# Kernel optimization log

Measured on AMD Instinct MI355X. Metric: run time of the kernel, lower is better.

The kernel has to match this reference:

```python
import jax, jax.numpy as jnp
import numpy as np

N_NODES = 100000
N_EDGES = 3200000
N_FEAT = 500
N_HID = 256
N_CLASS = 40


def spmm(edge_row, edge_col, edge_val, x, num_nodes):
    # out[i] = sum_{e: row[e]==i} val[e] * x[col[e]]
    msgs = edge_val[:, None] * x[edge_col]          # [E, F] gather + scale
    return jax.ops.segment_sum(msgs, edge_row, num_segments=num_nodes)


def setup_inputs() -> dict:
    key = jax.random.key(0)
    k1, k2, k3, k4, k5, k6, k7, k8 = jax.random.split(key, 8)
    features = jax.random.normal(k1, (N_NODES, N_FEAT), dtype=jnp.float32)
    edge_row = jax.random.randint(k2, (N_EDGES,), 0, N_NODES, dtype=jnp.int32)
    edge_col = jax.random.randint(k3, (N_EDGES,), 0, N_NODES, dtype=jnp.int32)
    edge_val = jax.random.uniform(k4, (N_EDGES,), dtype=jnp.float32)
    # Xavier-uniform linear weights, zero biases (as in reset_parameters)
    lim1 = float(np.sqrt(6.0 / (N_FEAT + N_HID)))
    W1 = jax.random.uniform(k5, (N_FEAT, N_HID), minval=-lim1, maxval=lim1, dtype=jnp.float32)
    b1 = jnp.zeros((N_HID,), dtype=jnp.float32)
    lim2 = float(np.sqrt(6.0 / (N_HID + N_CLASS)))
    W2 = jax.random.uniform(k6, (N_HID, N_CLASS), minval=-lim2, maxval=lim2, dtype=jnp.float32)
    b2 = jnp.zeros((N_CLASS,), dtype=jnp.float32)
    return {
        "features": features,
        "edge_row": edge_row,
        "edge_col": edge_col,
        "edge_val": edge_val,
        "W1": W1, "b1": b1, "W2": W2, "b2": b2,
    }


def reference(features, edge_row, edge_col, edge_val, W1, b1, W2, b2):
    # Layer 1: linear -> spmm -> relu   (eval mode: dropout is identity)
    h = features @ W1 + b1                          # [N, nhid]
    h = spmm(edge_row, edge_col, edge_val, h, N_NODES)
    h = jax.nn.relu(h)
    # Layer 2: linear -> spmm
    o = h @ W2 + b2                                 # [N, nclass]
    o = spmm(edge_row, edge_col, edge_val, o, N_NODES)
    return jax.nn.log_softmax(o, axis=1)
```

## Files before the change

kernel.cpp:

```cpp
#include <hip/hip_runtime.h>
#include <hip/hip_bf16.h>
#include <math.h>

#define N_NODES 100000
#define N_FEAT 500
#define N_HID 256
#define N_CLASS 40

typedef float f32x4 __attribute__((ext_vector_type(4)));
typedef short short8 __attribute__((ext_vector_type(8)));
typedef unsigned short u16x8 __attribute__((ext_vector_type(8)));

__device__ __forceinline__ float b2f(unsigned short u) {
  union { unsigned int i; float f; } c; c.i = ((unsigned int)u) << 16; return c.f;
}
__device__ __forceinline__ unsigned short f2bu(float x) {
  __hip_bfloat16 b = __float2bfloat16(x);
  union { __hip_bfloat16 b; unsigned short u; } c; c.b = b; return c.u;
}
__device__ __forceinline__ void gload_lds16(const void* gptr, void* lptr) {
  __builtin_amdgcn_global_load_lds(
      (const __attribute__((address_space(1))) unsigned int*)gptr,
      (__attribute__((address_space(3))) unsigned int*)lptr, 16, 0, 0);
}

__global__ __launch_bounds__(256) void cast_w1(
    const float* __restrict__ W1, unsigned short* __restrict__ Bsw) {
  int t = blockIdx.x * 256 + threadIdx.x;
  int col = t >> 6, ch = t & 63;
  int g = ch >> 3, c = ch & 7;
  int c_src = c ^ (col & 7);
  int k = g * 64 + c_src * 8;
  u16x8 o;
#pragma unroll
  for (int j = 0; j < 8; j++) {
    int kk = k + j;
    o[j] = (kk < N_FEAT) ? f2bu(W1[(size_t)kk * N_HID + col]) : (unsigned short)0;
  }
  *(u16x8*)(Bsw + (size_t)col * 512 + g * 64 + c * 8) = o;
}

__global__ __launch_bounds__(512) void gemm1_mfma(
    const float* __restrict__ A, const unsigned short* __restrict__ Bsw,
    const float* __restrict__ b1, unsigned short* __restrict__ H, int M) {
  __shared__ __align__(16) char smem[49152];
  char* sA = smem;
  char* sB = smem + 16384;
  int tid = threadIdx.x;
  int lane = tid & 63, w = tid >> 6;
  int wr = w >> 2, wc = w & 3;
  int bm = blockIdx.x * 128;

  f32x4 acc[4][4];
#pragma unroll
  for (int m = 0; m < 4; m++)
#pragma unroll
    for (int n = 0; n < 4; n++) acc[m][n] = (f32x4)0.f;

  for (int s = 0; s < 8; s++) {
    int k0 = s * 64;
#pragma unroll
    for (int i = 0; i < 4; i++) {
      int f4 = i * 512 + tid;
      int row = f4 >> 4, cidx = f4 & 15;
      int grow = bm + row;
      int k = k0 + cidx * 4;
      float4 v = make_float4(0.f, 0.f, 0.f, 0.f);
      if (grow < M && k < N_FEAT) v = *(const float4*)(A + (size_t)grow * N_FEAT + k);
      ushort4 u;
      u.x = f2bu(v.x); u.y = f2bu(v.y); u.z = f2bu(v.z); u.w = f2bu(v.w);
      int chunk = cidx >> 1, sub = cidx & 1;
      int byte = row * 128 + (((chunk ^ (row & 7))) << 4) + (sub << 3);
      *(ushort4*)(sA + byte) = u;
    }
#pragma unroll
    for (int j = 0; j < 4; j++) {
      int base = j * 8192 + w * 1024;
      int L = base + lane * 16;
      int col = L >> 7, c = (L >> 4) & 7;
      const char* g = (const char*)Bsw + (size_t)col * 1024 + s * 128 + c * 16;
      gload_lds16(g, sB + base);
    }
    __syncthreads();
#pragma unroll
    for (int kk = 0; kk < 2; kk++) {
      int cw = kk * 4 + (lane >> 4);
      short8 af[4], bg[4];
#pragma unroll
      for (int m = 0; m < 4; m++) {
        int ar = wr * 64 + m * 16 + (lane & 15);
        af[m] = *(const short8*)(sA + ar * 128 + ((cw ^ (ar & 7)) << 4));
      }
#pragma unroll
      for (int n = 0; n < 4; n++) {
        int bc = wc * 64 + n * 16 + (lane & 15);
        bg[n] = *(const short8*)(sB + bc * 128 + ((cw ^ (bc & 7)) << 4));
      }
#pragma unroll
      for (int m = 0; m < 4; m++)
#pragma unroll
        for (int n = 0; n < 4; n++)
          acc[m][n] = __builtin_amdgcn_mfma_f32_16x16x32_bf16(af[m], bg[n], acc[m][n], 0, 0, 0);
    }
    __syncthreads();
  }

  float bias[4];
#pragma unroll
  for (int n = 0; n < 4; n++) bias[n] = b1[wc * 64 + n * 16 + (lane & 15)];
#pragma unroll
  for (int m = 0; m < 4; m++) {
#pragma unroll
    for (int r = 0; r < 4; r++) {
      int row = bm + wr * 64 + m * 16 + ((lane >> 4) << 2) + r;
      if (row < M) {
#pragma unroll
        for (int n = 0; n < 4; n++) {
          int col = wc * 64 + n * 16 + (lane & 15);
          H[(size_t)row * N_HID + col] = f2bu(acc[m][n][r] + bias[n]);
        }
      }
    }
  }
}

__global__ __launch_bounds__(256) void hist_kernel(
    const int* __restrict__ er, int* __restrict__ cnt, int E) {
  int i = blockIdx.x * 256 + threadIdx.x;
  if (i < E) atomicAdd(&cnt[er[i]], 1);
}

__global__ __launch_bounds__(1024) void scan1_kernel(
    int* __restrict__ cnt, int* __restrict__ bsum, int n) {
  __shared__ int wsum[16];
  int tid = threadIdx.x, lane = tid & 63, wid = tid >> 6;
  int i = blockIdx.x * 1024 + tid;
  int v = (i < n) ? cnt[i] : 0;
  int x = v;
#pragma unroll
  for (int off = 1; off < 64; off <<= 1) {
    int t = __shfl_up(x, off);
    if (lane >= off) x += t;
  }
  if (lane == 63) wsum[wid] = x;
  __syncthreads();
  if (tid < 16) {
    int ws = wsum[tid];
#pragma unroll
    for (int off = 1; off < 16; off <<= 1) {
      int t = __shfl_up(ws, off);
      if (tid >= off) ws += t;
    }
    wsum[tid] = ws;
  }
  __syncthreads();
  int excl = (wid ? wsum[wid - 1] : 0) + x - v;
  if (i < n) cnt[i] = excl;
  if (tid == 0) bsum[blockIdx.x] = wsum[15];
}

__global__ __launch_bounds__(64) void scan2_kernel(
    int* __restrict__ bsum, int* __restrict__ row_ptr, int nb, int n) {
  int lane = threadIdx.x;
  int carry = 0;
  for (int base = 0; base < nb; base += 64) {
    int i = base + lane;
    int v = (i < nb) ? bsum[i] : 0;
    int x = v;
#pragma unroll
    for (int off = 1; off < 64; off <<= 1) {
      int t = __shfl_up(x, off);
      if (lane >= off) x += t;
    }
    if (i < nb) bsum[i] = carry + x - v;
    carry += __shfl(x, 63);
  }
  if (lane == 0) row_ptr[n] = carry;
}

__global__ __launch_bounds__(256) void scan3_kernel(
    int* __restrict__ cnt, const int* __restrict__ bsum,
    int* __restrict__ row_ptr, int n) {
  int i = blockIdx.x * 256 + threadIdx.x;
  if (i >= n) return;
  int v = cnt[i] + bsum[i >> 10];
  cnt[i] = v;
  row_ptr[i] = v;
}

__global__ __launch_bounds__(256) void scatter_kernel(
    const int* __restrict__ er, const int* __restrict__ ec,
    const float* __restrict__ ev, int* __restrict__ cursor,
    int2* __restrict__ cv, int E) {
  int i = blockIdx.x * 256 + threadIdx.x;
  if (i >= E) return;
  int r = er[i];
  int pos = atomicAdd(&cursor[r], 1);
  cv[pos] = make_int2(ec[i], __float_as_int(ev[i]));
}

__global__ __launch_bounds__(256) void spmm_csr_256(
    const int* __restrict__ row_ptr, const int2* __restrict__ cv,
    const unsigned short* __restrict__ X, unsigned short* __restrict__ Y, int M) {
  int wave = (blockIdx.x * 256 + threadIdx.x) >> 6;
  int lane = threadIdx.x & 63;
  if (wave >= M) return;
  int start = row_ptr[wave], end = row_ptr[wave + 1];
  float a0 = 0.f, a1 = 0.f, a2 = 0.f, a3 = 0.f;
  const unsigned short* Xl = X + (lane << 2);
  int e = start;
  for (; e + 4 <= end; e += 4) {
    int2 p0 = cv[e], p1 = cv[e + 1], p2 = cv[e + 2], p3 = cv[e + 3];
    ushort4 x0 = *(const ushort4*)(Xl + (size_t)p0.x * N_HID);
    ushort4 x1 = *(const ushort4*)(Xl + (size_t)p1.x * N_HID);
    ushort4 x2 = *(const ushort4*)(Xl + (size_t)p2.x * N_HID);
    ushort4 x3 = *(const ushort4*)(Xl + (size_t)p3.x * N_HID);
    float v0 = __int_as_float(p0.y), v1 = __int_as_float(p1.y);
    float v2 = __int_as_float(p2.y), v3 = __int_as_float(p3.y);
    a0 = fmaf(v0, b2f(x0.x), a0); a1 = fmaf(v0, b2f(x0.y), a1);
    a2 = fmaf(v0, b2f(x0.z), a2); a3 = fmaf(v0, b2f(x0.w), a3);
    a0 = fmaf(v1, b2f(x1.x), a0); a1 = fmaf(v1, b2f(x1.y), a1);
    a2 = fmaf(v1, b2f(x1.z), a2); a3 = fmaf(v1, b2f(x1.w), a3);
    a0 = fmaf(v2, b2f(x2.x), a0); a1 = fmaf(v2, b2f(x2.y), a1);
    a2 = fmaf(v2, b2f(x2.z), a2); a3 = fmaf(v2, b2f(x2.w), a3);
    a0 = fmaf(v3, b2f(x3.x), a0); a1 = fmaf(v3, b2f(x3.y), a1);
    a2 = fmaf(v3, b2f(x3.z), a2); a3 = fmaf(v3, b2f(x3.w), a3);
  }
  for (; e < end; e++) {
    int2 p0 = cv[e];
    float v0 = __int_as_float(p0.y);
    ushort4 x0 = *(const ushort4*)(Xl + (size_t)p0.x * N_HID);
    a0 = fmaf(v0, b2f(x0.x), a0); a1 = fmaf(v0, b2f(x0.y), a1);
    a2 = fmaf(v0, b2f(x0.z), a2); a3 = fmaf(v0, b2f(x0.w), a3);
  }
  ushort4 o;
  o.x = f2bu(fmaxf(a0, 0.f)); o.y = f2bu(fmaxf(a1, 0.f));
  o.z = f2bu(fmaxf(a2, 0.f)); o.w = f2bu(fmaxf(a3, 0.f));
  *(ushort4*)(Y + (size_t)wave * N_HID + (lane << 2)) = o;
}

__global__ __launch_bounds__(256) void gemm2_kernel(
    const unsigned short* __restrict__ H, const float* __restrict__ W2,
    const float* __restrict__ b2, unsigned short* __restrict__ O, int M) {
  __shared__ float Ws[N_HID * N_CLASS];
  __shared__ float sb2[N_CLASS];
  int tid = threadIdx.x;
  for (int i = tid; i < N_HID * N_CLASS; i += 256) Ws[i] = W2[i];
  if (tid < N_CLASS) sb2[tid] = b2[tid];
  __syncthreads();
  int r0 = (blockIdx.x * 256 + tid) * 2;
  if (r0 >= M) return;
  int r1 = r0 + 1;
  bool has1 = r1 < M;
  float acc0[N_CLASS], acc1[N_CLASS];
#pragma unroll
  for (int n = 0; n < N_CLASS; n++) { acc0[n] = sb2[n]; acc1[n] = sb2[n]; }
  const unsigned short* h0 = H + (size_t)r0 * N_HID;
  const unsigned short* h1 = H + (size_t)(has1 ? r1 : r0) * N_HID;
  for (int k0 = 0; k0 < N_HID; k0 += 8) {
    u16x8 va = *(const u16x8*)(h0 + k0);
    u16x8 vb = *(const u16x8*)(h1 + k0);
#pragma unroll
    for (int j = 0; j < 8; j++) {
      float a0 = b2f(va[j]), a1 = b2f(vb[j]);
      const float* wrow = &Ws[(k0 + j) * N_CLASS];
#pragma unroll
      for (int n = 0; n < N_CLASS; n++) {
        float wv = wrow[n];
        acc0[n] = fmaf(a0, wv, acc0[n]);
        acc1[n] = fmaf(a1, wv, acc1[n]);
      }
    }
  }
  unsigned short* o0 = O + (size_t)r0 * N_CLASS;
#pragma unroll
  for (int n = 0; n < N_CLASS; n += 4) {
    ushort4 p;
    p.x = f2bu(acc0[n]); p.y = f2bu(acc0[n + 1]);
    p.z = f2bu(acc0[n + 2]); p.w = f2bu(acc0[n + 3]);
    *(ushort4*)(o0 + n) = p;
  }
  if (has1) {
    unsigned short* o1 = O + (size_t)r1 * N_CLASS;
#pragma unroll
    for (int n = 0; n < N_CLASS; n += 4) {
      ushort4 p;
      p.x = f2bu(acc1[n]); p.y = f2bu(acc1[n + 1]);
      p.z = f2bu(acc1[n + 2]); p.w = f2bu(acc1[n + 3]);
      *(ushort4*)(o1 + n) = p;
    }
  }
}

__global__ __launch_bounds__(256) void spmm_csr_40_lsm(
    const int* __restrict__ row_ptr, const int2* __restrict__ cv,
    const unsigned short* __restrict__ X, float* __restrict__ Out, int M) {
  int wave = (blockIdx.x * 256 + threadIdx.x) >> 6;
  int lane = threadIdx.x & 63;
  if (wave >= M) return;
  int start = row_ptr[wave], end = row_ptr[wave + 1];
  bool act = lane < N_CLASS;
  int ln = act ? lane : 0;
  const unsigned short* Xc = X + ln;
  float acc = 0.f;
  int e = start;
  for (; e + 4 <= end; e += 4) {
    int2 p0 = cv[e], p1 = cv[e + 1], p2 = cv[e + 2], p3 = cv[e + 3];
    unsigned short x0 = Xc[(size_t)p0.x * N_CLASS];
    unsigned short x1 = Xc[(size_t)p1.x * N_CLASS];
    unsigned short x2 = Xc[(size_t)p2.x * N_CLASS];
    unsigned short x3 = Xc[(size_t)p3.x * N_CLASS];
    acc = fmaf(__int_as_float(p0.y), b2f(x0), acc);
    acc = fmaf(__int_as_float(p1.y), b2f(x1), acc);
    acc = fmaf(__int_as_float(p2.y), b2f(x2), acc);
    acc = fmaf(__int_as_float(p3.y), b2f(x3), acc);
  }
  for (; e < end; e++) {
    int2 p0 = cv[e];
    acc = fmaf(__int_as_float(p0.y), b2f(Xc[(size_t)p0.x * N_CLASS]), acc);
  }
  float mv = act ? acc : -INFINITY;
#pragma unroll
  for (int off = 32; off; off >>= 1) mv = fmaxf(mv, __shfl_xor(mv, off));
  float ex = act ? expf(acc - mv) : 0.f;
  float s = ex;
#pragma unroll
  for (int off = 32; off; off >>= 1) s += __shfl_xor(s, off);
  float lse = mv + logf(s);
  if (act) Out[(size_t)wave * N_CLASS + lane] = acc - lse;
}

extern "C" void kernel_launch(void* const* d_in, const int* in_sizes, int n_in,
                              void* d_out, int out_size, void* d_ws, size_t ws_size,
                              hipStream_t stream) {
  const float* feat = (const float*)d_in[0];
  const int* er     = (const int*)d_in[1];
  const int* ec     = (const int*)d_in[2];
  const float* ev   = (const float*)d_in[3];
  const float* W1   = (const float*)d_in[4];
  const float* b1   = (const float*)d_in[5];
  const float* W2   = (const float*)d_in[6];
  const float* b2   = (const float*)d_in[7];
  float* out = (float*)d_out;
  const int M = N_NODES;
  const int E = in_sizes[1];

  char* ws = (char*)d_ws;
  unsigned short* h     = (unsigned short*)(ws);
  unsigned short* hpost = (unsigned short*)(ws + 51200000);
  unsigned short* o     = (unsigned short*)(ws + 102400000);
  int* row_ptr          = (int*)(ws + 110400000);
  int* cursor           = (int*)(ws + 110800016);
  int* bsum             = (int*)(ws + 111200032);
  int2* cv              = (int2*)(ws + 111200576);
  unsigned short* W1Tsw = (unsigned short*)(ws + 136800576);

  const int NB1 = (M + 1023) / 1024;

  cast_w1<<<64, 256, 0, stream>>>(W1, W1Tsw);
  hipMemsetAsync(cursor, 0, (size_t)M * sizeof(int), stream);
  hist_kernel<<<(E + 255) / 256, 256, 0, stream>>>(er, cursor, E);
  scan1_kernel<<<NB1, 1024, 0, stream>>>(cursor, bsum, M);
  scan2_kernel<<<1, 64, 0, stream>>>(bsum, row_ptr, NB1, M);
  scan3_kernel<<<(M + 255) / 256, 256, 0, stream>>>(cursor, bsum, row_ptr, M);
  scatter_kernel<<<(E + 255) / 256, 256, 0, stream>>>(er, ec, ev, cursor, cv, E);
  gemm1_mfma<<<(M + 127) / 128, 512, 0, stream>>>(feat, W1Tsw, b1, h, M);
  spmm_csr_256<<<(M + 3) / 4, 256, 0, stream>>>(row_ptr, cv, h, hpost, M);
  gemm2_kernel<<<(M + 511) / 512, 256, 0, stream>>>(hpost, W2, b2, o, M);
  spmm_csr_40_lsm<<<(M + 3) / 4, 256, 0, stream>>>(row_ptr, cv, o, out, M);
}
```

Baseline: 795.7 us.

## Vectorize histogram and partition CSR scatter by row slice across block groups

The histogram kernel becomes a grid-stride loop over 4-wide nontemporal loads of edge rows. The scatter kernel splits its 2048 blocks into 8 slices selected by bits 9-11 of the row index. Every slice reads the whole edge list, but each block only does atomics and cv writes for rows in its own slice, which is meant to keep cursor atomics and scattered writes more localized. The cost is reading the edge arrays eight times and more divergent work per thread.

```diff
diff --git a/kernel.cpp b/kernel.cpp
--- a/kernel.cpp
+++ b/kernel.cpp
@@ -8,6 +8,7 @@
 #define N_CLASS 40
 
 typedef float f32x4 __attribute__((ext_vector_type(4)));
+typedef int i32x4 __attribute__((ext_vector_type(4)));
 typedef short short8 __attribute__((ext_vector_type(8)));
 typedef unsigned short u16x8 __attribute__((ext_vector_type(8)));
 
@@ -126,8 +127,20 @@
 
 __global__ __launch_bounds__(256) void hist_kernel(
     const int* __restrict__ er, int* __restrict__ cnt, int E) {
-  int i = blockIdx.x * 256 + threadIdx.x;
-  if (i < E) atomicAdd(&cnt[er[i]], 1);
+  int nv = E >> 2;
+  int t = blockIdx.x * 256 + threadIdx.x;
+  int nthr = gridDim.x * 256;
+  const i32x4* er4 = (const i32x4*)er;
+  for (int i = t; i < nv; i += nthr) {
+    i32x4 r = __builtin_nontemporal_load(&er4[i]);
+    atomicAdd(&cnt[r.x], 1);
+    atomicAdd(&cnt[r.y], 1);
+    atomicAdd(&cnt[r.z], 1);
+    atomicAdd(&cnt[r.w], 1);
+  }
+  int tail = nv << 2;
+  if (blockIdx.x == 0 && threadIdx.x < E - tail)
+    atomicAdd(&cnt[er[tail + threadIdx.x]], 1);
 }
 
 __global__ __launch_bounds__(1024) void scan1_kernel(
@@ -192,11 +205,43 @@
     const int* __restrict__ er, const int* __restrict__ ec,
     const float* __restrict__ ev, int* __restrict__ cursor,
     int2* __restrict__ cv, int E) {
-  int i = blockIdx.x * 256 + threadIdx.x;
-  if (i >= E) return;
-  int r = er[i];
-  int pos = atomicAdd(&cursor[r], 1);
-  cv[pos] = make_int2(ec[i], __float_as_int(ev[i]));
+  int s = blockIdx.x & 7;
+  int g = blockIdx.x >> 3;
+  int ngrp = gridDim.x >> 3;
+  int t = g * 256 + threadIdx.x;
+  int nthr = ngrp * 256;
+  int nv = E >> 2;
+  const i32x4* er4 = (const i32x4*)er;
+  const i32x4* ec4 = (const i32x4*)ec;
+  const f32x4* ev4 = (const f32x4*)ev;
+  for (int i = t; i < nv; i += nthr) {
+    i32x4 r = __builtin_nontemporal_load(&er4[i]);
+    i32x4 c = __builtin_nontemporal_load(&ec4[i]);
+    f32x4 v = __builtin_nontemporal_load(&ev4[i]);
+    if (((r.x >> 9) & 7) == s) {
+      int p = atomicAdd(&cursor[r.x], 1);
+      cv[p] = make_int2(c.x, __float_as_int(v.x));
+    }
+    if (((r.y >> 9) & 7) == s) {
+      int p = atomicAdd(&cursor[r.y], 1);
+      cv[p] = make_int2(c.y, __float_as_int(v.y));
+    }
+    if (((r.z >> 9) & 7) == s) {
+      int p = atomicAdd(&cursor[r.z], 1);
+      cv[p] = make_int2(c.z, __float_as_int(v.z));
+    }
+    if (((r.w >> 9) & 7) == s) {
+      int p = atomicAdd(&cursor[r.w], 1);
+      cv[p] = make_int2(c.w, __float_as_int(v.w));
+    }
+  }
+  int tail = nv << 2;
+  if (blockIdx.x == 0 && threadIdx.x < E - tail) {
+    int i = tail + threadIdx.x;
+    int row = er[i];
+    int p = atomicAdd(&cursor[row], 1);
+    cv[p] = make_int2(ec[i], __float_as_int(ev[i]));
+  }
 }
 
 __global__ __launch_bounds__(256) void spmm_csr_256(
@@ -358,12 +403,12 @@
   const int NB1 = (M + 1023) / 1024;
 
   cast_w1<<<64, 256, 0, stream>>>(W1, W1Tsw);
-  hipMemsetAsync(cursor, 0, (size_t)M * sizeof(int), stream);
-  hist_kernel<<<(E + 255) / 256, 256, 0, stream>>>(er, cursor, E);
+  (void)hipMemsetAsync(cursor, 0, (size_t)M * sizeof(int), stream);
+  hist_kernel<<<1024, 256, 0, stream>>>(er, cursor, E);
   scan1_kernel<<<NB1, 1024, 0, stream>>>(cursor, bsum, M);
   scan2_kernel<<<1, 64, 0, stream>>>(bsum, row_ptr, NB1, M);
   scan3_kernel<<<(M + 255) / 256, 256, 0, stream>>>(cursor, bsum, row_ptr, M);
-  scatter_kernel<<<(E + 255) / 256, 256, 0, stream>>>(er, ec, ev, cursor, cv, E);
+  scatter_kernel<<<2048, 256, 0, stream>>>(er, ec, ev, cursor, cv, E);
   gemm1_mfma<<<(M + 127) / 128, 512, 0, stream>>>(feat, W1Tsw, b1, h, M);
   spmm_csr_256<<<(M + 3) / 4, 256, 0, stream>>>(row_ptr, cv, h, hpost, M);
   gemm2_kernel<<<(M + 511) / 512, 256, 0, stream>>>(hpost, W2, b2, o, M);
```

Result: no change. 789.9 us (-0.7%).
